# Kernel tuning notes

Hardware: AMD Instinct MI355X
Metric: run time of the kernel (lower is better)

The kernel has to match this reference:

```python
import jax, jax.numpy as jnp
import numpy as np

B, C, T, H, W = 4, 1024, 8, 16, 16
CI = 512  # inter_channels = C // 2
EPS = 1e-5


def setup_inputs() -> dict:
    key = jax.random.key(0)
    ks = jax.random.split(key, 8)
    s = 0.02
    return {
        "x": jax.random.normal(ks[0], (B, C, T, H, W), dtype=jnp.float32),
        "g_w": jax.random.normal(ks[1], (CI, C), dtype=jnp.float32) * s,
        "g_b": jnp.zeros((CI,), jnp.float32),
        "theta_w": jax.random.normal(ks[2], (CI, C), dtype=jnp.float32) * s,
        "theta_b": jnp.zeros((CI,), jnp.float32),
        "phi_w": jax.random.normal(ks[3], (CI, C), dtype=jnp.float32) * s,
        "phi_b": jnp.zeros((CI,), jnp.float32),
        "w_w": jax.random.normal(ks[4], (C, CI), dtype=jnp.float32) * s,
        "w_b": jnp.zeros((C,), jnp.float32),
        "bn_gamma": jnp.ones((C,), jnp.float32),
        "bn_beta": jnp.zeros((C,), jnp.float32),
    }


def reference(x, g_w, g_b, theta_w, theta_b, phi_w, phi_b, w_w, w_b, bn_gamma, bn_beta):
    b, c, t, h, w = x.shape
    xf = x.reshape(b, c, -1)  # (b, c, n), n = t*h*w
    # 1x1x1 convs == per-token linear projections
    g_x = jnp.einsum('oc,bcn->bno', g_w, xf) + g_b            # (b, n, ci)
    theta_x = jnp.einsum('oc,bcn->bno', theta_w, xf) + theta_b  # (b, n, ci)
    phi_x = jnp.einsum('oc,bcn->bon', phi_w, xf) + phi_b[None, :, None]  # (b, ci, n)
    f = jnp.einsum('bni,bim->bnm', theta_x, phi_x)            # (b, n, n)
    attn = jax.nn.softmax(f, axis=-1)                         # instance == 'soft'
    y = jnp.einsum('bnm,bmo->bon', attn, g_x)                 # (b, ci, n)
    w_y = jnp.einsum('co,bon->bcn', w_w, y) + w_b[None, :, None]  # (b, c, n)
    # BatchNorm3d (training mode): normalize over (batch, spatial) per channel
    mean = w_y.mean(axis=(0, 2), keepdims=True)
    var = w_y.var(axis=(0, 2), keepdims=True)
    w_y = (w_y - mean) * jax.lax.rsqrt(var + EPS)
    w_y = w_y * bn_gamma[None, :, None] + bn_beta[None, :, None]
    z = w_y + xf
    return z.reshape(b, c, t, h, w)
```

## Files before the change

kernel.cpp:

```cpp
#include <hip/hip_runtime.h>
#include <hip/hip_bf16.h>

#define B_   4
#define C_   1024
#define CI_  512
#define NSP_ 2048
#define EPS_ 1e-5f

typedef _Float16 f16x8 __attribute__((ext_vector_type(8)));
typedef float f32x4  __attribute__((ext_vector_type(4)));
typedef unsigned short ushort_t;

static __device__ inline ushort_t f2h(float v) {
    _Float16 h = (_Float16)v;
    ushort_t u;
    __builtin_memcpy(&u, &h, 2);
    return u;
}

template<bool OUT_F16>
__global__ __launch_bounds__(256, 2)
void gemm_tn(const ushort_t* __restrict__ A, const ushort_t* __restrict__ Bm,
             void* __restrict__ Cout,
             const float* __restrict__ biasM, const float* __restrict__ biasN,
             int N, int K, int lda, int ldb, int ldc,
             long sA, long sB, long sC)
{
    __shared__ ushort_t smA[128 * 32];
    __shared__ ushort_t smB[128 * 32];
    const int bz = blockIdx.z;
    const ushort_t* Ag = A + bz * sA;
    const ushort_t* Bg = Bm + bz * sB;
    const int m0 = blockIdx.y * 128;
    const int n0 = blockIdx.x * 128;
    const int tid  = threadIdx.x;
    const int wave = tid >> 6;
    const int lane = tid & 63;
    const int wm = wave >> 1, wn = wave & 1;
    const int fr = lane & 15;
    const int kg = lane >> 4;

    int offA[2], offB[2];
    #pragma unroll
    for (int t = 0; t < 2; ++t) {
        const int s   = (wave * 2 + t) * 64 + lane;
        const int row = s >> 2;
        const int kc  = s & 3;
        offA[t] = (m0 + row) * lda + kc * 8;
        offB[t] = (n0 + row) * ldb + kc * 8;
    }
    int aoff[4], boff[4];
    #pragma unroll
    for (int i = 0; i < 4; ++i) {
        aoff[i] = (wm * 64 + i * 16 + fr) * 32 + kg * 8;
        boff[i] = (wn * 64 + i * 16 + fr) * 32 + kg * 8;
    }

    f32x4 acc[4][4];
    #pragma unroll
    for (int i = 0; i < 4; ++i)
        #pragma unroll
        for (int j = 0; j < 4; ++j)
            acc[i][j] = (f32x4)0.f;

    for (int k0 = 0; k0 < K; k0 += 32) {
        #pragma unroll
        for (int t = 0; t < 2; ++t) {
            __builtin_amdgcn_global_load_lds(
                (const __attribute__((address_space(1))) void*)(Ag + offA[t] + k0),
                (__attribute__((address_space(3))) void*)(&smA[(wave * 2 + t) * 512]),
                16, 0, 0);
            __builtin_amdgcn_global_load_lds(
                (const __attribute__((address_space(1))) void*)(Bg + offB[t] + k0),
                (__attribute__((address_space(3))) void*)(&smB[(wave * 2 + t) * 512]),
                16, 0, 0);
        }
        __syncthreads();

        f16x8 aF[4], bF[4];
        #pragma unroll
        for (int i = 0; i < 4; ++i) aF[i] = *(const f16x8*)&smA[aoff[i]];
        #pragma unroll
        for (int j = 0; j < 4; ++j) bF[j] = *(const f16x8*)&smB[boff[j]];
        #pragma unroll
        for (int i = 0; i < 4; ++i)
            #pragma unroll
            for (int j = 0; j < 4; ++j)
                acc[i][j] = __builtin_amdgcn_mfma_f32_16x16x32_f16(aF[i], bF[j], acc[i][j], 0, 0, 0);
        __syncthreads();
    }

    float*    Cf = (float*)Cout + bz * sC;
    ushort_t* Ch = (ushort_t*)Cout + bz * sC;
    #pragma unroll
    for (int i = 0; i < 4; ++i) {
        const int growb = m0 + wm * 64 + i * 16 + kg * 4;
        #pragma unroll
        for (int j = 0; j < 4; ++j) {
            const int gcol = n0 + wn * 64 + j * 16 + fr;
            const float bN = biasN ? biasN[gcol] : 0.f;
            #pragma unroll
            for (int r = 0; r < 4; ++r) {
                const int grow = growb + r;
                float v = acc[i][j][r] + bN + (biasM ? biasM[grow] : 0.f);
                if (OUT_F16) Ch[(long)grow * ldc + gcol] = f2h(v);
                else         Cf[(long)grow * ldc + gcol] = v;
            }
        }
    }
}

__global__ __launch_bounds__(256)
void transpose_cvt(const float* __restrict__ x, ushort_t* __restrict__ xT)
{
    __shared__ ushort_t t[64][65];
    const int b  = blockIdx.z;
    const int n0 = blockIdx.x * 64, c0 = blockIdx.y * 64;
    const float*  xp = x  + ((long)b * C_ + c0) * NSP_ + n0;
    ushort_t*     op = xT + ((long)b * NSP_ + n0) * C_ + c0;
    const int tr = threadIdx.x >> 6;
    const int tc = threadIdx.x & 63;
    #pragma unroll
    for (int i = 0; i < 16; ++i) {
        const int row = tr * 16 + i;
        t[row][tc] = f2h(xp[(long)row * NSP_ + tc]);
    }
    __syncthreads();
    #pragma unroll
    for (int i = 0; i < 16; ++i) {
        const int row = tr * 16 + i;
        op[(long)row * C_ + tc] = t[tc][row];
    }
}

struct U4 { ushort_t a, b, c, d; };
__global__ __launch_bounds__(256)
void cvt4(const float* __restrict__ in, ushort_t* __restrict__ out, int n4)
{
    const int i = blockIdx.x * 256 + threadIdx.x;
    if (i < n4) {
        const float4 v = ((const float4*)in)[i];
        U4 u{f2h(v.x), f2h(v.y), f2h(v.z), f2h(v.w)};
        ((U4*)out)[i] = u;
    }
}

__global__ __launch_bounds__(256)
void concat_bias(const float* __restrict__ a, const float* __restrict__ b, float* __restrict__ o)
{
    const int i = blockIdx.x * 256 + threadIdx.x;
    if (i < CI_)            o[i] = a[i];
    else if (i < 2 * CI_)   o[i] = b[i - CI_];
}

__global__ __launch_bounds__(256)
void softmax2048(const float* __restrict__ f, ushort_t* __restrict__ attn)
{
    const long rid = blockIdx.x;
    const float* p = f + rid * NSP_;
    ushort_t*    o = attn + rid * (2 * NSP_);
    const int tid = threadIdx.x;
    float v[8];
    #pragma unroll
    for (int i = 0; i < 8; ++i) v[i] = p[tid + (i << 8)];
    float mx = v[0];
    #pragma unroll
    for (int i = 1; i < 8; ++i) mx = fmaxf(mx, v[i]);

    __shared__ float red[256];
    red[tid] = mx;
    __syncthreads();
    for (int s = 128; s > 0; s >>= 1) {
        if (tid < s) red[tid] = fmaxf(red[tid], red[tid + s]);
        __syncthreads();
    }
    mx = red[0];
    __syncthreads();

    float sum = 0.f;
    #pragma unroll
    for (int i = 0; i < 8; ++i) { v[i] = __expf(v[i] - mx); sum += v[i]; }
    red[tid] = sum;
    __syncthreads();
    for (int s = 128; s > 0; s >>= 1) {
        if (tid < s) red[tid] += red[tid + s];
        __syncthreads();
    }
    const float inv = 1.f / red[0];
    __syncthreads();
    #pragma unroll
    for (int i = 0; i < 8; ++i) o[tid + (i << 8)] = f2h(v[i] * inv);
}

__global__ __launch_bounds__(256)
void bn_stats(const float* __restrict__ wy, const float* __restrict__ gamma,
              const float* __restrict__ beta, float* __restrict__ scale,
              float* __restrict__ shift)
{
    const int c = blockIdx.x;
    const int tid = threadIdx.x;
    float s = 0.f, q = 0.f;
    for (int b = 0; b < B_; ++b) {
        const float* p = wy + ((long)b * C_ + c) * NSP_;
        #pragma unroll
        for (int i = 0; i < NSP_ / 256; ++i) {
            const float v = p[tid + (i << 8)];
            s += v; q += v * v;
        }
    }
    __shared__ float rs[256], rq[256];
    rs[tid] = s; rq[tid] = q;
    __syncthreads();
    for (int st = 128; st > 0; st >>= 1) {
        if (tid < st) { rs[tid] += rs[tid + st]; rq[tid] += rq[tid + st]; }
        __syncthreads();
    }
    if (tid == 0) {
        const float inv = 1.f / (float)(B_ * NSP_);
        const float mean = rs[0] * inv;
        const float var  = rq[0] * inv - mean * mean;
        const float sc = rsqrtf(var + EPS_) * gamma[c];
        scale[c] = sc;
        shift[c] = beta[c] - mean * sc;
    }
}

__global__ __launch_bounds__(256)
void bn_apply(const float* __restrict__ wy, const float* __restrict__ x,
              const float* __restrict__ scale, const float* __restrict__ shift,
              float* __restrict__ out)
{
    const long total4 = (long)B_ * C_ * NSP_ / 4;
    for (long i = (long)blockIdx.x * 256 + threadIdx.x; i < total4;
         i += (long)gridDim.x * 256) {
        const int c = (int)((i >> 9) & (C_ - 1));
        const float4 w  = ((const float4*)wy)[i];
        const float4 xv = ((const float4*)x)[i];
        const float sc = scale[c], sh = shift[c];
        float4 o;
        o.x = w.x * sc + sh + xv.x;
        o.y = w.y * sc + sh + xv.y;
        o.z = w.z * sc + sh + xv.z;
        o.w = w.w * sc + sh + xv.w;
        ((float4*)out)[i] = o;
    }
}

extern "C" void kernel_launch(void* const* d_in, const int* in_sizes, int n_in,
                              void* d_out, int out_size, void* d_ws, size_t ws_size,
                              hipStream_t stream)
{
    const float* x     = (const float*)d_in[0];
    const float* g_w   = (const float*)d_in[1];
    const float* g_b   = (const float*)d_in[2];
    const float* th_w  = (const float*)d_in[3];
    const float* th_b  = (const float*)d_in[4];
    const float* ph_w  = (const float*)d_in[5];
    const float* ph_b  = (const float*)d_in[6];
    const float* w_w   = (const float*)d_in[7];
    const float* w_b   = (const float*)d_in[8];
    const float* gamma = (const float*)d_in[9];
    const float* beta  = (const float*)d_in[10];
    float* out = (float*)d_out;
    char*  ws  = (char*)d_ws;

    ushort_t* xT      = (ushort_t*)(ws + 0);
    ushort_t* tw      = (ushort_t*)(ws + 16777216);
    ushort_t* g_w_h   = (ushort_t*)(ws + 18874368);
    ushort_t* w_w_h   = (ushort_t*)(ws + 19922944);
    ushort_t* thph    = (ushort_t*)(ws + 20971520);
    ushort_t* gcn     = (ushort_t*)(ws + 37748736);
    float*    f       = (float*)   (ws + 46137344);
    float*    bias_tp = (float*)   (ws + 113246208);
    float*    scale   = (float*)   (ws + 113250304);
    float*    shift   = (float*)   (ws + 113254400);

    ushort_t* y    = thph;
    ushort_t* attn = (ushort_t*)f;
    float*    wy   = f;

    const dim3 blk(256);

    transpose_cvt<<<dim3(NSP_ / 64, C_ / 64, B_), blk, 0, stream>>>(x, xT);

    cvt4<<<512, blk, 0, stream>>>(th_w, tw,          131072);
    cvt4<<<512, blk, 0, stream>>>(ph_w, tw + 524288, 131072);
    cvt4<<<512, blk, 0, stream>>>(g_w,  g_w_h,       131072);
    cvt4<<<512, blk, 0, stream>>>(w_w,  w_w_h,       131072);
    concat_bias<<<4, blk, 0, stream>>>(th_b, ph_b, bias_tp);

    gemm_tn<true><<<dim3(1024 / 128, NSP_ / 128, B_), blk, 0, stream>>>(
        xT, tw, thph, nullptr, bias_tp,
        1024, C_, C_, C_, 1024, (long)NSP_ * C_, 0, (long)NSP_ * 1024);

    gemm_tn<true><<<dim3(NSP_ / 128, CI_ / 128, B_), blk, 0, stream>>>(
        g_w_h, xT, gcn, g_b, nullptr,
        NSP_, C_, C_, C_, NSP_, 0, (long)NSP_ * C_, (long)CI_ * NSP_);

    gemm_tn<false><<<dim3(NSP_ / 128, NSP_ / 128, B_), blk, 0, stream>>>(
        thph, thph + CI_, f, nullptr, nullptr,
        NSP_, CI_, 1024, 1024, NSP_,
        (long)NSP_ * 1024, (long)NSP_ * 1024, (long)NSP_ * NSP_);

    softmax2048<<<B_ * NSP_, blk, 0, stream>>>(f, attn);

    gemm_tn<true><<<dim3(CI_ / 128, NSP_ / 128, B_), blk, 0, stream>>>(
        attn, gcn, y, nullptr, nullptr,
        CI_, NSP_, 2 * NSP_, NSP_, CI_,
        (long)NSP_ * 2 * NSP_, (long)CI_ * NSP_, (long)NSP_ * CI_);

    gemm_tn<false><<<dim3(NSP_ / 128, C_ / 128, B_), blk, 0, stream>>>(
        w_w_h, y, wy, w_b, nullptr,
        NSP_, CI_, CI_, CI_, NSP_, 0, (long)NSP_ * CI_, (long)C_ * NSP_);

    bn_stats<<<C_, blk, 0, stream>>>(wy, gamma, beta, scale, shift);
    bn_apply<<<2048, blk, 0, stream>>>(wy, x, scale, shift, out);
}
```

Measured before the change: 320.9 us.

## Store scores and projection output in fp16, split-K attn GEMM, fuse BN stats

Attention scores and the final projection output are now written in fp16 instead of fp32, which roughly halves traffic for softmax, BN stats and BN apply. The attn×g GEMM uses a 2-way split-K with fp32 partials that a new combine kernel adds together, raising block count for a grid that was small. BN sums are accumulated inside the last GEMM epilogue with shuffles and atomics, which replaces the separate stats pass over the output. The cost is lower precision in the scores and the BN input, extra partial-buffer traffic, and float atomics that make the statistics order-dependent.

```diff
diff --git a/kernel.cpp b/kernel.cpp
--- a/kernel.cpp
+++ b/kernel.cpp
@@ -17,20 +17,28 @@
     __builtin_memcpy(&u, &h, 2);
     return u;
 }
-
-template<bool OUT_F16>
+static __device__ inline float h2f(ushort_t u) {
+    _Float16 h;
+    __builtin_memcpy(&h, &u, 2);
+    return (float)h;
+}
+
+template<bool OUT_F16, int KSPLIT, bool STATS>
 __global__ __launch_bounds__(256, 2)
 void gemm_tn(const ushort_t* __restrict__ A, const ushort_t* __restrict__ Bm,
              void* __restrict__ Cout,
              const float* __restrict__ biasM, const float* __restrict__ biasN,
              int N, int K, int lda, int ldb, int ldc,
-             long sA, long sB, long sC)
+             long sA, long sB, long sC, long sK,
+             float* __restrict__ sums, float* __restrict__ sumsq)
 {
     __shared__ ushort_t smA[128 * 32];
     __shared__ ushort_t smB[128 * 32];
-    const int bz = blockIdx.z;
-    const ushort_t* Ag = A + bz * sA;
-    const ushort_t* Bg = Bm + bz * sB;
+    const int bz = blockIdx.z / KSPLIT;
+    const int ks = blockIdx.z % KSPLIT;
+    const int Ksub = K / KSPLIT;
+    const ushort_t* Ag = A + bz * sA + (long)ks * Ksub;
+    const ushort_t* Bg = Bm + bz * sB + (long)ks * Ksub;
     const int m0 = blockIdx.y * 128;
     const int n0 = blockIdx.x * 128;
     const int tid  = threadIdx.x;
@@ -63,7 +71,7 @@
         for (int j = 0; j < 4; ++j)
             acc[i][j] = (f32x4)0.f;
 
-    for (int k0 = 0; k0 < K; k0 += 32) {
+    for (int k0 = 0; k0 < Ksub; k0 += 32) {
         #pragma unroll
         for (int t = 0; t < 2; ++t) {
             __builtin_amdgcn_global_load_lds(
@@ -90,21 +98,34 @@
         __syncthreads();
     }
 
-    float*    Cf = (float*)Cout + bz * sC;
-    ushort_t* Ch = (ushort_t*)Cout + bz * sC;
+    float*    Cf = (float*)Cout + bz * sC + ks * sK;
+    ushort_t* Ch = (ushort_t*)Cout + bz * sC + ks * sK;
     #pragma unroll
     for (int i = 0; i < 4; ++i) {
-        const int growb = m0 + wm * 64 + i * 16 + kg * 4;
-        #pragma unroll
-        for (int j = 0; j < 4; ++j) {
-            const int gcol = n0 + wn * 64 + j * 16 + fr;
-            const float bN = biasN ? biasN[gcol] : 0.f;
+        #pragma unroll
+        for (int r = 0; r < 4; ++r) {
+            const int grow = m0 + wm * 64 + i * 16 + kg * 4 + r;
+            const float bM = biasM ? biasM[grow] : 0.f;
+            float s = 0.f, q = 0.f;
             #pragma unroll
-            for (int r = 0; r < 4; ++r) {
-                const int grow = growb + r;
-                float v = acc[i][j][r] + bN + (biasM ? biasM[grow] : 0.f);
+            for (int j = 0; j < 4; ++j) {
+                const int gcol = n0 + wn * 64 + j * 16 + fr;
+                const float bN = biasN ? biasN[gcol] : 0.f;
+                const float v = acc[i][j][r] + bN + bM;
                 if (OUT_F16) Ch[(long)grow * ldc + gcol] = f2h(v);
                 else         Cf[(long)grow * ldc + gcol] = v;
+                if (STATS) { s += v; q += v * v; }
+            }
+            if (STATS) {
+                #pragma unroll
+                for (int m = 1; m < 16; m <<= 1) {
+                    s += __shfl_xor(s, m, 64);
+                    q += __shfl_xor(q, m, 64);
+                }
+                if (fr == 0) {
+                    atomicAdd(&sums[grow], s);
+                    atomicAdd(&sumsq[grow], q);
+                }
             }
         }
     }
@@ -154,15 +175,17 @@
 }
 
 __global__ __launch_bounds__(256)
-void softmax2048(const float* __restrict__ f, ushort_t* __restrict__ attn)
+void softmax2048(const ushort_t* __restrict__ fh, ushort_t* __restrict__ attn)
 {
     const long rid = blockIdx.x;
-    const float* p = f + rid * NSP_;
-    ushort_t*    o = attn + rid * (2 * NSP_);
     const int tid = threadIdx.x;
+    const uint4 w = ((const uint4*)(fh + rid * NSP_))[tid];
+    ushort_t h[8];
+    __builtin_memcpy(h, &w, 16);
     float v[8];
     #pragma unroll
-    for (int i = 0; i < 8; ++i) v[i] = p[tid + (i << 8)];
+    for (int i = 0; i < 8; ++i) v[i] = h2f(h[i]);
+
     float mx = v[0];
     #pragma unroll
     for (int i = 1; i < 8; ++i) mx = fmaxf(mx, v[i]);
@@ -187,38 +210,40 @@
         __syncthreads();
     }
     const float inv = 1.f / red[0];
-    __syncthreads();
-    #pragma unroll
-    for (int i = 0; i < 8; ++i) o[tid + (i << 8)] = f2h(v[i] * inv);
-}
-
-__global__ __launch_bounds__(256)
-void bn_stats(const float* __restrict__ wy, const float* __restrict__ gamma,
-              const float* __restrict__ beta, float* __restrict__ scale,
-              float* __restrict__ shift)
-{
-    const int c = blockIdx.x;
-    const int tid = threadIdx.x;
-    float s = 0.f, q = 0.f;
-    for (int b = 0; b < B_; ++b) {
-        const float* p = wy + ((long)b * C_ + c) * NSP_;
-        #pragma unroll
-        for (int i = 0; i < NSP_ / 256; ++i) {
-            const float v = p[tid + (i << 8)];
-            s += v; q += v * v;
-        }
-    }
-    __shared__ float rs[256], rq[256];
-    rs[tid] = s; rq[tid] = q;
-    __syncthreads();
-    for (int st = 128; st > 0; st >>= 1) {
-        if (tid < st) { rs[tid] += rs[tid + st]; rq[tid] += rq[tid + st]; }
-        __syncthreads();
-    }
-    if (tid == 0) {
+    #pragma unroll
+    for (int i = 0; i < 8; ++i) h[i] = f2h(v[i] * inv);
+    uint4 wo;
+    __builtin_memcpy(&wo, h, 16);
+    ((uint4*)(attn + rid * NSP_))[tid] = wo;
+}
+
+__global__ __launch_bounds__(256)
+void combine2(const float* __restrict__ p0, const float* __restrict__ p1,
+              ushort_t* __restrict__ out)
+{
+    const long i = (long)blockIdx.x * 256 + threadIdx.x;
+    const float4 a0 = ((const float4*)p0)[2 * i];
+    const float4 a1 = ((const float4*)p0)[2 * i + 1];
+    const float4 b0 = ((const float4*)p1)[2 * i];
+    const float4 b1 = ((const float4*)p1)[2 * i + 1];
+    ushort_t h[8] = {
+        f2h(a0.x + b0.x), f2h(a0.y + b0.y), f2h(a0.z + b0.z), f2h(a0.w + b0.w),
+        f2h(a1.x + b1.x), f2h(a1.y + b1.y), f2h(a1.z + b1.z), f2h(a1.w + b1.w)};
+    uint4 wo;
+    __builtin_memcpy(&wo, h, 16);
+    ((uint4*)out)[i] = wo;
+}
+
+__global__ __launch_bounds__(256)
+void bn_finalize(const float* __restrict__ sums, const float* __restrict__ sumsq,
+                 const float* __restrict__ gamma, const float* __restrict__ beta,
+                 float* __restrict__ scale, float* __restrict__ shift)
+{
+    const int c = blockIdx.x * 256 + threadIdx.x;
+    if (c < C_) {
         const float inv = 1.f / (float)(B_ * NSP_);
-        const float mean = rs[0] * inv;
-        const float var  = rq[0] * inv - mean * mean;
+        const float mean = sums[c] * inv;
+        const float var  = sumsq[c] * inv - mean * mean;
         const float sc = rsqrtf(var + EPS_) * gamma[c];
         scale[c] = sc;
         shift[c] = beta[c] - mean * sc;
@@ -226,23 +251,31 @@
 }
 
 __global__ __launch_bounds__(256)
-void bn_apply(const float* __restrict__ wy, const float* __restrict__ x,
+void bn_apply(const ushort_t* __restrict__ wy, const float* __restrict__ x,
               const float* __restrict__ scale, const float* __restrict__ shift,
               float* __restrict__ out)
 {
-    const long total4 = (long)B_ * C_ * NSP_ / 4;
-    for (long i = (long)blockIdx.x * 256 + threadIdx.x; i < total4;
+    const long total8 = (long)B_ * C_ * NSP_ / 8;
+    for (long i = (long)blockIdx.x * 256 + threadIdx.x; i < total8;
          i += (long)gridDim.x * 256) {
-        const int c = (int)((i >> 9) & (C_ - 1));
-        const float4 w  = ((const float4*)wy)[i];
-        const float4 xv = ((const float4*)x)[i];
+        const int c = (int)((i >> 8) & (C_ - 1));
+        const uint4 ww = ((const uint4*)wy)[i];
+        ushort_t h[8];
+        __builtin_memcpy(h, &ww, 16);
+        const float4 x0 = ((const float4*)x)[2 * i];
+        const float4 x1 = ((const float4*)x)[2 * i + 1];
         const float sc = scale[c], sh = shift[c];
-        float4 o;
-        o.x = w.x * sc + sh + xv.x;
-        o.y = w.y * sc + sh + xv.y;
-        o.z = w.z * sc + sh + xv.z;
-        o.w = w.w * sc + sh + xv.w;
-        ((float4*)out)[i] = o;
+        float4 o0, o1;
+        o0.x = h2f(h[0]) * sc + sh + x0.x;
+        o0.y = h2f(h[1]) * sc + sh + x0.y;
+        o0.z = h2f(h[2]) * sc + sh + x0.z;
+        o0.w = h2f(h[3]) * sc + sh + x0.w;
+        o1.x = h2f(h[4]) * sc + sh + x1.x;
+        o1.y = h2f(h[5]) * sc + sh + x1.y;
+        o1.z = h2f(h[6]) * sc + sh + x1.z;
+        o1.w = h2f(h[7]) * sc + sh + x1.w;
+        ((float4*)out)[2 * i]     = o0;
+        ((float4*)out)[2 * i + 1] = o1;
     }
 }
 
@@ -270,14 +303,17 @@
     ushort_t* w_w_h   = (ushort_t*)(ws + 19922944);
     ushort_t* thph    = (ushort_t*)(ws + 20971520);
     ushort_t* gcn     = (ushort_t*)(ws + 37748736);
-    float*    f       = (float*)   (ws + 46137344);
-    float*    bias_tp = (float*)   (ws + 113246208);
-    float*    scale   = (float*)   (ws + 113250304);
-    float*    shift   = (float*)   (ws + 113254400);
-
+    ushort_t* fh      = (ushort_t*)(ws + 46137344);
+    ushort_t* attn    = (ushort_t*)(ws + 79691776);
+    float*    bias_tp = (float*)   (ws + 111149056);
+    float*    sums    = (float*)   (ws + 111153152);
+    float*    sumsq   = (float*)   (ws + 111157248);
+    float*    scale   = (float*)   (ws + 111161344);
+    float*    shift   = (float*)   (ws + 111165440);
+
+    float*    yp   = (float*)fh;
     ushort_t* y    = thph;
-    ushort_t* attn = (ushort_t*)f;
-    float*    wy   = f;
+    ushort_t* wy   = attn;
 
     const dim3 blk(256);
 
@@ -288,31 +324,40 @@
     cvt4<<<512, blk, 0, stream>>>(g_w,  g_w_h,       131072);
     cvt4<<<512, blk, 0, stream>>>(w_w,  w_w_h,       131072);
     concat_bias<<<4, blk, 0, stream>>>(th_b, ph_b, bias_tp);
-
-    gemm_tn<true><<<dim3(1024 / 128, NSP_ / 128, B_), blk, 0, stream>>>(
+    hipMemsetAsync(sums,  0, C_ * sizeof(float), stream);
+    hipMemsetAsync(sumsq, 0, C_ * sizeof(float), stream);
+
+    gemm_tn<true, 1, false><<<dim3(1024 / 128, NSP_ / 128, B_), blk, 0, stream>>>(
         xT, tw, thph, nullptr, bias_tp,
-        1024, C_, C_, C_, 1024, (long)NSP_ * C_, 0, (long)NSP_ * 1024);
-
-    gemm_tn<true><<<dim3(NSP_ / 128, CI_ / 128, B_), blk, 0, stream>>>(
+        1024, C_, C_, C_, 1024, (long)NSP_ * C_, 0, (long)NSP_ * 1024, 0,
+        nullptr, nullptr);
+
+    gemm_tn<true, 1, false><<<dim3(NSP_ / 128, CI_ / 128, B_), blk, 0, stream>>>(
         g_w_h, xT, gcn, g_b, nullptr,
-        NSP_, C_, C_, C_, NSP_, 0, (long)NSP_ * C_, (long)CI_ * NSP_);
-
-    gemm_tn<false><<<dim3(NSP_ / 128, NSP_ / 128, B_), blk, 0, stream>>>(
-        thph, thph + CI_, f, nullptr, nullptr,
+        NSP_, C_, C_, C_, NSP_, 0, (long)NSP_ * C_, (long)CI_ * NSP_, 0,
+        nullptr, nullptr);
+
+    gemm_tn<true, 1, false><<<dim3(NSP_ / 128, NSP_ / 128, B_), blk, 0, stream>>>(
+        thph, thph + CI_, fh, nullptr, nullptr,
         NSP_, CI_, 1024, 1024, NSP_,
-        (long)NSP_ * 1024, (long)NSP_ * 1024, (long)NSP_ * NSP_);
-
-    softmax2048<<<B_ * NSP_, blk, 0, stream>>>(f, attn);
-
-    gemm_tn<true><<<dim3(CI_ / 128, NSP_ / 128, B_), blk, 0, stream>>>(
-        attn, gcn, y, nullptr, nullptr,
-        CI_, NSP_, 2 * NSP_, NSP_, CI_,
-        (long)NSP_ * 2 * NSP_, (long)CI_ * NSP_, (long)NSP_ * CI_);
-
-    gemm_tn<false><<<dim3(NSP_ / 128, C_ / 128, B_), blk, 0, stream>>>(
+        (long)NSP_ * 1024, (long)NSP_ * 1024, (long)NSP_ * NSP_, 0,
+        nullptr, nullptr);
+
+    softmax2048<<<B_ * NSP_, blk, 0, stream>>>(fh, attn);
+
+    gemm_tn<false, 2, false><<<dim3(CI_ / 128, NSP_ / 128, B_ * 2), blk, 0, stream>>>(
+        attn, gcn, yp, nullptr, nullptr,
+        CI_, NSP_, NSP_, NSP_, CI_,
+        (long)NSP_ * NSP_, (long)CI_ * NSP_, (long)NSP_ * CI_,
+        (long)B_ * NSP_ * CI_, nullptr, nullptr);
+
+    combine2<<<8192, blk, 0, stream>>>(yp, yp + (long)B_ * NSP_ * CI_, y);
+
+    gemm_tn<true, 1, true><<<dim3(NSP_ / 128, C_ / 128, B_), blk, 0, stream>>>(
         w_w_h, y, wy, w_b, nullptr,
-        NSP_, CI_, CI_, CI_, NSP_, 0, (long)NSP_ * CI_, (long)C_ * NSP_);
-
-    bn_stats<<<C_, blk, 0, stream>>>(wy, gamma, beta, scale, shift);
+        NSP_, CI_, CI_, CI_, NSP_, 0, (long)NSP_ * CI_, (long)C_ * NSP_, 0,
+        sums, sumsq);
+
+    bn_finalize<<<4, blk, 0, stream>>>(sums, sumsq, gamma, beta, scale, shift);
     bn_apply<<<2048, blk, 0, stream>>>(wy, x, scale, shift, out);
 }
```

After: 331.0 us. +3.1%, slower.
